# Kernel optimization log

Hardware: AMD Instinct MI355X
Metric: run time of the kernel (lower is better)

## Reference

```python
import jax, jax.numpy as jnp
import numpy as np
from jax import lax

SHIFT_SIZE = 5
PAD = SHIFT_SIZE // 2


def _chunk_shifts(C):
    # torch.chunk(x, 5, dim=1): chunk size = ceil(C/5); shift for chunk i is i - PAD
    csz = -(-C // SHIFT_SIZE)
    return jnp.arange(C) // csz - PAD  # (C,) in [-PAD, PAD]


def _shift_along_h(x, shifts):
    # x: (B,C,H,W). Equivalent of pad+chunk+roll(dim=2)+cat+narrow: per-channel
    # zero-filled shift along H (no wraparound since |shift| <= PAD).
    B, C, H, W = x.shape
    xp = jnp.pad(x, ((0, 0), (0, 0), (PAD, PAD), (0, 0)))
    c_idx = jnp.arange(C)[:, None]              # (C,1)
    h_idx = jnp.arange(H)[None, :] + PAD - shifts[:, None]  # (C,H)
    return xp[:, c_idx, h_idx, :]               # (B,C,H,W)


def _shift_along_w(x, shifts):
    return jnp.swapaxes(_shift_along_h(jnp.swapaxes(x, 2, 3), shifts), 2, 3)


def setup_inputs() -> dict:
    key = jax.random.key(0)
    ks = jax.random.split(key, 7)
    B, H, W, C, hidden = 8, 128, 128, 256, 256
    x = jax.random.normal(ks[0], (B, H * W, C), dtype=jnp.float32)
    w1 = jax.random.normal(ks[1], (hidden, C), dtype=jnp.float32) * 0.02
    b1 = jnp.zeros((hidden,), dtype=jnp.float32)
    fan_out = 3 * 3 * hidden // hidden  # groups = hidden
    dw_w = jax.random.normal(ks[2], (hidden, 1, 3, 3), dtype=jnp.float32) * np.sqrt(2.0 / fan_out)
    dw_b = jnp.zeros((hidden,), dtype=jnp.float32)
    w2 = jax.random.normal(ks[3], (C, hidden), dtype=jnp.float32) * 0.02
    b2 = jnp.zeros((C,), dtype=jnp.float32)
    return {"x": x, "H": H, "W": W, "w1": w1, "b1": b1,
            "dw_w": dw_w, "dw_b": dw_b, "w2": w2, "b2": b2}


def reference(x, H, W, w1, b1, dw_w, dw_b, w2, b2):
    B, N, C = x.shape
    shifts = _chunk_shifts(C)

    # --- shift along H, then fc1 ---
    xn = jnp.reshape(jnp.swapaxes(x, 1, 2), (B, C, H, W))
    x_s = _shift_along_h(xn, shifts)
    x_s = jnp.swapaxes(x_s.reshape(B, C, H * W), 1, 2)   # (B,N,C)
    h = x_s @ w1.T + b1                                  # (B,N,hidden)

    # --- depthwise 3x3 conv ---
    Ch = h.shape[-1]
    himg = jnp.reshape(jnp.swapaxes(h, 1, 2), (B, Ch, H, W))
    himg = lax.conv_general_dilated(
        himg, dw_w, window_strides=(1, 1), padding=((1, 1), (1, 1)),
        feature_group_count=Ch,
        dimension_numbers=("NCHW", "OIHW", "NCHW")) + dw_b[None, :, None, None]
    h = jnp.swapaxes(himg.reshape(B, Ch, H * W), 1, 2)

    h = jax.nn.gelu(h, approximate=False)

    # --- shift along W, then fc2 ---
    hn = jnp.reshape(jnp.swapaxes(h, 1, 2), (B, Ch, H, W))
    h_s = _shift_along_w(hn, _chunk_shifts(Ch))
    h_s = jnp.swapaxes(h_s.reshape(B, Ch, H * W), 1, 2)  # (B,N,hidden)
    out = h_s @ w2.T + b2                                # (B,N,C)
    return out
```

## Files before the change

### kernel.cpp

```cpp
#include <hip/hip_runtime.h>
#include <hip/hip_bf16.h>
#include <math.h>

#define Hc   128
#define Wc   128
#define Cc   256
#define Nc   (Hc * Wc)
#define Bn   8
#define Mtot (Bn * Nc)
#define CSZ  52
#define SPAD 2

typedef unsigned short ushort4v __attribute__((ext_vector_type(4)));
typedef unsigned short ushort8  __attribute__((ext_vector_type(8)));
typedef __bf16         bf16x8   __attribute__((ext_vector_type(8)));
typedef float          f32x4    __attribute__((ext_vector_type(4)));

__device__ __forceinline__ float bf2f(unsigned short u) {
    return __uint_as_float(((unsigned)u) << 16);
}
__device__ __forceinline__ unsigned short f2bf(float f) {
    unsigned u = __float_as_uint(f);
    return (unsigned short)((u + 0x7fffu + ((u >> 16) & 1u)) >> 16);
}
__device__ __forceinline__ unsigned pk2bf(float a, float b) {
    unsigned ua = __float_as_uint(a) + 0x8000u;
    unsigned ub = __float_as_uint(b) + 0x8000u;
    return __builtin_amdgcn_perm(ub, ua, 0x07060302);
}
__device__ __forceinline__ void async16(const void* g, void* l) {
    __builtin_amdgcn_global_load_lds(
        (const __attribute__((address_space(1))) unsigned*)g,
        (__attribute__((address_space(3))) unsigned*)l, 16, 0, 0);
}

__global__ __launch_bounds__(256)
void prep_xshift_kernel(const float* __restrict__ x, unsigned short* __restrict__ xs)
{
    const int gid = blockIdx.x * 256 + threadIdx.x;
    const int grp = gid & 63;
    const int nl  = gid >> 6;
    const int c0  = grp * 4;
    const int s   = c0 / CSZ - SPAD;
    const int h   = (nl & (Nc - 1)) >> 7;
    const int hs  = h - s;
    float4 v = make_float4(0.f, 0.f, 0.f, 0.f);
    if (hs >= 0 && hs < Hc) v = *(const float4*)(x + ((size_t)nl - s * Wc) * Cc + c0);
    ushort4v o = { f2bf(v.x), f2bf(v.y), f2bf(v.z), f2bf(v.w) };
    *(ushort4v*)(xs + (size_t)nl * Cc + c0) = o;
}

__global__ __launch_bounds__(256)
void fc1_mfma_kernel(const unsigned short* __restrict__ A, const float* __restrict__ w1,
                     const float* __restrict__ b1, unsigned short* __restrict__ h1)
{
    __shared__ __bf16 As[128 * 32];
    __shared__ __bf16 Bs[128 * 32];
    __shared__ __align__(16) unsigned short Cs[128 * 136];

    const int tid  = threadIdx.x;
    const int lane = tid & 63;
    const int wave = tid >> 6;
    const int wm = (wave >> 1) * 64, wn = (wave & 1) * 64;
    const size_t m0 = (size_t)blockIdx.x * 128;
    const int j0 = blockIdx.y * 128;

    const int idx0 = tid, idx1 = tid + 256;
    const int brow = tid >> 1, bch = (tid & 1) * 16;

    f32x4 acc[4][4] = {};
    for (int k0 = 0; k0 < Cc; k0 += 32) {
        async16(A + (m0 + (idx0 >> 2)) * Cc + k0 + (idx0 & 3) * 8, As + idx0 * 8);
        async16(A + (m0 + (idx1 >> 2)) * Cc + k0 + (idx1 & 3) * 8, As + idx1 * 8);
        {
            const float* src = w1 + (size_t)(j0 + brow) * Cc + k0 + bch;
            float4 v0 = *(const float4*)(src);
            float4 v1 = *(const float4*)(src + 4);
            float4 v2 = *(const float4*)(src + 8);
            float4 v3 = *(const float4*)(src + 12);
            uint4 p0, p1;
            p0.x = pk2bf(v0.x, v0.y); p0.y = pk2bf(v0.z, v0.w);
            p0.z = pk2bf(v1.x, v1.y); p0.w = pk2bf(v1.z, v1.w);
            p1.x = pk2bf(v2.x, v2.y); p1.y = pk2bf(v2.z, v2.w);
            p1.z = pk2bf(v3.x, v3.y); p1.w = pk2bf(v3.z, v3.w);
            *(uint4*)(Bs + brow * 32 + bch)     = p0;
            *(uint4*)(Bs + brow * 32 + bch + 8) = p1;
        }
        __syncthreads();
        bf16x8 a[4], b[4];
        const int kq = (lane >> 4) * 8;
        const int r  = lane & 15;
#pragma unroll
        for (int i = 0; i < 4; ++i) {
            a[i] = *(const bf16x8*)(As + (wm + i * 16 + r) * 32 + kq);
            b[i] = *(const bf16x8*)(Bs + (wn + i * 16 + r) * 32 + kq);
        }
#pragma unroll
        for (int i = 0; i < 4; ++i)
#pragma unroll
            for (int j = 0; j < 4; ++j)
                acc[i][j] = __builtin_amdgcn_mfma_f32_16x16x32_bf16(a[i], b[j], acc[i][j], 0, 0, 0);
        __syncthreads();
    }

    const int cq = (lane >> 4) * 4;
    const int cc = lane & 15;
    float bv[4];
#pragma unroll
    for (int j = 0; j < 4; ++j) bv[j] = b1[j0 + wn + j * 16 + cc];
#pragma unroll
    for (int i = 0; i < 4; ++i)
#pragma unroll
        for (int j = 0; j < 4; ++j) {
            const int col = wn + j * 16 + cc;
#pragma unroll
            for (int rg = 0; rg < 4; ++rg)
                Cs[(wm + i * 16 + cq + rg) * 136 + col] = f2bf(acc[i][j][rg] + bv[j]);
        }
    __syncthreads();
    {
        const int row = tid >> 1, half = tid & 1;
        const unsigned short* src = Cs + row * 136 + half * 64;
        unsigned short* dst = h1 + (m0 + row) * Cc + j0 + half * 64;
#pragma unroll
        for (int i = 0; i < 8; ++i)
            *(uint4*)(dst + i * 8) = *(const uint4*)(src + i * 8);
    }
}

__global__ __launch_bounds__(256)
void zero_borders_kernel(unsigned short* __restrict__ gsh)
{
    const int gid = blockIdx.x * 256 + threadIdx.x;
    const int cg  = gid & 31;
    const int rest = gid >> 5;
    const int wi = rest & 3;
    const int bh = rest >> 2;
    const int w  = (wi & 2) ? (wi + 124) : wi;
    uint4 z; z.x = z.y = z.z = z.w = 0u;
    *(uint4*)(gsh + ((size_t)bh * 128 + w) * Cc + cg * 8) = z;
}

__global__ __launch_bounds__(256)
void dwconv_gelu_scatter_kernel(const unsigned short* __restrict__ h1,
                                const float* __restrict__ dw_w, const float* __restrict__ dw_b,
                                unsigned short* __restrict__ gsh)
{
    __shared__ float wsm[9][256];
    for (int i = threadIdx.x; i < 9 * 256; i += 256) {
        const int tap = i % 9, c = i / 9;
        wsm[tap][(c >> 3) | ((c & 7) << 5)] = dw_w[i];
    }
    __syncthreads();

    const int n_lin = blockIdx.x * 8 + (threadIdx.x >> 5);
    const int li = threadIdx.x & 31;
    const int cg = li * 8;
    const int b = n_lin >> 14;
    const int n = n_lin & (Nc - 1);
    const int hh = n >> 7, ww = n & 127;
    const size_t bN = (size_t)b * Nc;

    float acc[8];
#pragma unroll
    for (int c = 0; c < 8; ++c) acc[c] = dw_b[cg + c];

#pragma unroll
    for (int dy = -1; dy <= 1; ++dy) {
        const int y = hh + dy;
        if (y < 0 || y >= Hc) continue;
#pragma unroll
        for (int dx = -1; dx <= 1; ++dx) {
            const int xw = ww + dx;
            if (xw < 0 || xw >= Wc) continue;
            const int tap = (dy + 1) * 3 + (dx + 1);
            const ushort8 raw = *(const ushort8*)(h1 + (bN + y * Wc + xw) * Cc + cg);
#pragma unroll
            for (int c = 0; c < 8; ++c)
                acc[c] += bf2f(raw[c]) * wsm[tap][li | (c << 5)];
        }
    }

    unsigned short ov[8];
#pragma unroll
    for (int c = 0; c < 8; ++c) {
        const float v = acc[c];
        ov[c] = f2bf(0.5f * v * (1.0f + erff(v * 0.70710678118654752f)));
    }
    const int s0 = cg / CSZ - SPAD;
    const int s1 = (cg + 4) / CSZ - SPAD;
    const int w0 = ww + s0, w1 = ww + s1;
    if ((unsigned)w0 < (unsigned)Wc) {
        ushort4v t = { ov[0], ov[1], ov[2], ov[3] };
        *(ushort4v*)(gsh + (bN + hh * Wc + w0) * Cc + cg) = t;
    }
    if ((unsigned)w1 < (unsigned)Wc) {
        ushort4v t = { ov[4], ov[5], ov[6], ov[7] };
        *(ushort4v*)(gsh + (bN + hh * Wc + w1) * Cc + cg + 4) = t;
    }
}

__global__ __launch_bounds__(256)
void fc2_mfma_kernel(const unsigned short* __restrict__ A, const float* __restrict__ w2,
                     const float* __restrict__ b2, float* __restrict__ out)
{
    __shared__ __bf16 As[128 * 32];
    __shared__ __bf16 Bs[128 * 32];

    const int tid  = threadIdx.x;
    const int lane = tid & 63;
    const int wave = tid >> 6;
    const int wm = (wave >> 1) * 64, wn = (wave & 1) * 64;
    const size_t m0 = (size_t)blockIdx.x * 128;
    const int j0 = blockIdx.y * 128;

    const int idx0 = tid, idx1 = tid + 256;
    const int brow = tid >> 1, bch = (tid & 1) * 16;

    f32x4 acc[4][4] = {};
    for (int k0 = 0; k0 < Cc; k0 += 32) {
        async16(A + (m0 + (idx0 >> 2)) * Cc + k0 + (idx0 & 3) * 8, As + idx0 * 8);
        async16(A + (m0 + (idx1 >> 2)) * Cc + k0 + (idx1 & 3) * 8, As + idx1 * 8);
        {
            const float* src = w2 + (size_t)(j0 + brow) * Cc + k0 + bch;
            float4 v0 = *(const float4*)(src);
            float4 v1 = *(const float4*)(src + 4);
            float4 v2 = *(const float4*)(src + 8);
            float4 v3 = *(const float4*)(src + 12);
            uint4 p0, p1;
            p0.x = pk2bf(v0.x, v0.y); p0.y = pk2bf(v0.z, v0.w);
            p0.z = pk2bf(v1.x, v1.y); p0.w = pk2bf(v1.z, v1.w);
            p1.x = pk2bf(v2.x, v2.y); p1.y = pk2bf(v2.z, v2.w);
            p1.z = pk2bf(v3.x, v3.y); p1.w = pk2bf(v3.z, v3.w);
            *(uint4*)(Bs + brow * 32 + bch)     = p0;
            *(uint4*)(Bs + brow * 32 + bch + 8) = p1;
        }
        __syncthreads();
        bf16x8 a[4], b[4];
        const int kq = (lane >> 4) * 8;
        const int r  = lane & 15;
#pragma unroll
        for (int i = 0; i < 4; ++i) {
            a[i] = *(const bf16x8*)(As + (wm + i * 16 + r) * 32 + kq);
            b[i] = *(const bf16x8*)(Bs + (wn + i * 16 + r) * 32 + kq);
        }
#pragma unroll
        for (int i = 0; i < 4; ++i)
#pragma unroll
            for (int j = 0; j < 4; ++j)
                acc[i][j] = __builtin_amdgcn_mfma_f32_16x16x32_bf16(a[i], b[j], acc[i][j], 0, 0, 0);
        __syncthreads();
    }

    const int cq = (lane >> 4) * 4;
    const int cc = lane & 15;
    float bv[4];
#pragma unroll
    for (int j = 0; j < 4; ++j) bv[j] = b2[j0 + wn + j * 16 + cc];
#pragma unroll
    for (int i = 0; i < 4; ++i)
#pragma unroll
        for (int j = 0; j < 4; ++j) {
            const int col = j0 + wn + j * 16 + cc;
#pragma unroll
            for (int rg = 0; rg < 4; ++rg)
                out[(m0 + wm + i * 16 + cq + rg) * Cc + col] = acc[i][j][rg] + bv[j];
        }
}

extern "C" void kernel_launch(void* const* d_in, const int* in_sizes, int n_in,
                              void* d_out, int out_size, void* d_ws, size_t ws_size,
                              hipStream_t stream) {
    const float* x    = (const float*)d_in[0];
    const float* w1   = (const float*)d_in[3];
    const float* b1   = (const float*)d_in[4];
    const float* dw_w = (const float*)d_in[5];
    const float* dw_b = (const float*)d_in[6];
    const float* w2   = (const float*)d_in[7];
    const float* b2   = (const float*)d_in[8];
    float* out = (float*)d_out;

    unsigned short* xs  = (unsigned short*)d_ws;
    unsigned short* h1  = xs + (size_t)Mtot * Cc;
    unsigned short* gsh = xs;

    prep_xshift_kernel<<<dim3(Mtot * 64 / 256), dim3(256), 0, stream>>>(x, xs);
    fc1_mfma_kernel<<<dim3(Mtot / 128, 2), dim3(256), 0, stream>>>(xs, w1, b1, h1);
    zero_borders_kernel<<<dim3(512), dim3(256), 0, stream>>>(gsh);
    dwconv_gelu_scatter_kernel<<<dim3(Mtot / 8), dim3(256), 0, stream>>>(h1, dw_w, dw_b, gsh);
    fc2_mfma_kernel<<<dim3(Mtot / 128, 2), dim3(256), 0, stream>>>(gsh, w2, b2, out);
}
```

Before: 418.9 us.

## Fuse H-shift into fc1 A-load, register-block dwconv, and use fast GELU

Drops the separate x-shift prep pass. fc1 now loads fp32 x directly with the per-channel H shift and converts it to bf16 while staging the A tile. A small prep kernel converts w1 to bf16 and transposes the depthwise weights into scratch space inside the output buffer, so fc1 can stream its weights asynchronously. The depthwise conv now computes 4 adjacent output pixels per thread to reuse loaded input columns, and replaces erf-GELU with a tanh-style approximation built from exp and rcp. That approximation changes numerics slightly relative to exact GELU.

Result: faster. 388.5 us (-7.3%).

```diff
diff --git a/kernel.cpp b/kernel.cpp
--- a/kernel.cpp
+++ b/kernel.cpp
@@ -35,23 +35,20 @@
 }
 
 __global__ __launch_bounds__(256)
-void prep_xshift_kernel(const float* __restrict__ x, unsigned short* __restrict__ xs)
-{
-    const int gid = blockIdx.x * 256 + threadIdx.x;
-    const int grp = gid & 63;
-    const int nl  = gid >> 6;
-    const int c0  = grp * 4;
-    const int s   = c0 / CSZ - SPAD;
-    const int h   = (nl & (Nc - 1)) >> 7;
-    const int hs  = h - s;
-    float4 v = make_float4(0.f, 0.f, 0.f, 0.f);
-    if (hs >= 0 && hs < Hc) v = *(const float4*)(x + ((size_t)nl - s * Wc) * Cc + c0);
-    ushort4v o = { f2bf(v.x), f2bf(v.y), f2bf(v.z), f2bf(v.w) };
-    *(ushort4v*)(xs + (size_t)nl * Cc + c0) = o;
-}
-
-__global__ __launch_bounds__(256)
-void fc1_mfma_kernel(const unsigned short* __restrict__ A, const float* __restrict__ w1,
+void wprep_kernel(const float* __restrict__ w1, const float* __restrict__ dw_w,
+                  unsigned short* __restrict__ w1b, float* __restrict__ dwT)
+{
+    const int g = blockIdx.x * 256 + threadIdx.x;
+    {
+        float4 a = *(const float4*)(w1 + (size_t)g * 4);
+        ushort4v o = { f2bf(a.x), f2bf(a.y), f2bf(a.z), f2bf(a.w) };
+        *(ushort4v*)(w1b + (size_t)g * 4) = o;
+    }
+    if (g < 9 * Cc) dwT[(g % 9) * Cc + g / 9] = dw_w[g];
+}
+
+__global__ __launch_bounds__(256)
+void fc1_mfma_kernel(const float* __restrict__ x, const unsigned short* __restrict__ w1b,
                      const float* __restrict__ b1, unsigned short* __restrict__ h1)
 {
     __shared__ __bf16 As[128 * 32];
@@ -62,38 +59,45 @@
     const int lane = tid & 63;
     const int wave = tid >> 6;
     const int wm = (wave >> 1) * 64, wn = (wave & 1) * 64;
-    const size_t m0 = (size_t)blockIdx.x * 128;
+    const int bx = blockIdx.x;
+    const size_t m0 = (size_t)bx * 128;
     const int j0 = blockIdx.y * 128;
-
+    const int bb = bx >> 7, hh = bx & 127;
+    const int r = tid >> 1, half = tid & 1;
     const int idx0 = tid, idx1 = tid + 256;
-    const int brow = tid >> 1, bch = (tid & 1) * 16;
 
     f32x4 acc[4][4] = {};
     for (int k0 = 0; k0 < Cc; k0 += 32) {
-        async16(A + (m0 + (idx0 >> 2)) * Cc + k0 + (idx0 & 3) * 8, As + idx0 * 8);
-        async16(A + (m0 + (idx1 >> 2)) * Cc + k0 + (idx1 & 3) * 8, As + idx1 * 8);
+        async16(w1b + (size_t)(j0 + (idx0 >> 2)) * Cc + k0 + (idx0 & 3) * 8, Bs + idx0 * 8);
+        async16(w1b + (size_t)(j0 + (idx1 >> 2)) * Cc + k0 + (idx1 & 3) * 8, Bs + idx1 * 8);
         {
-            const float* src = w1 + (size_t)(j0 + brow) * Cc + k0 + bch;
-            float4 v0 = *(const float4*)(src);
-            float4 v1 = *(const float4*)(src + 4);
-            float4 v2 = *(const float4*)(src + 8);
-            float4 v3 = *(const float4*)(src + 12);
-            uint4 p0, p1;
-            p0.x = pk2bf(v0.x, v0.y); p0.y = pk2bf(v0.z, v0.w);
-            p0.z = pk2bf(v1.x, v1.y); p0.w = pk2bf(v1.z, v1.w);
-            p1.x = pk2bf(v2.x, v2.y); p1.y = pk2bf(v2.z, v2.w);
-            p1.z = pk2bf(v3.x, v3.y); p1.w = pk2bf(v3.z, v3.w);
-            *(uint4*)(Bs + brow * 32 + bch)     = p0;
-            *(uint4*)(Bs + brow * 32 + bch + 8) = p1;
+            const int kb = k0 + half * 16;
+            unsigned p[8];
+#pragma unroll
+            for (int j = 0; j < 4; ++j) {
+                const int c  = kb + j * 4;
+                const int s  = c / CSZ - SPAD;
+                const int hs = hh - s;
+                float4 v = make_float4(0.f, 0.f, 0.f, 0.f);
+                if (hs >= 0 && hs < Hc)
+                    v = *(const float4*)(x + ((size_t)(bb * Nc + hs * Wc + r)) * Cc + c);
+                p[j * 2]     = pk2bf(v.x, v.y);
+                p[j * 2 + 1] = pk2bf(v.z, v.w);
+            }
+            uint4 q0, q1;
+            q0.x = p[0]; q0.y = p[1]; q0.z = p[2]; q0.w = p[3];
+            q1.x = p[4]; q1.y = p[5]; q1.z = p[6]; q1.w = p[7];
+            *(uint4*)(As + r * 32 + half * 16)     = q0;
+            *(uint4*)(As + r * 32 + half * 16 + 8) = q1;
         }
         __syncthreads();
         bf16x8 a[4], b[4];
         const int kq = (lane >> 4) * 8;
-        const int r  = lane & 15;
+        const int rr = lane & 15;
 #pragma unroll
         for (int i = 0; i < 4; ++i) {
-            a[i] = *(const bf16x8*)(As + (wm + i * 16 + r) * 32 + kq);
-            b[i] = *(const bf16x8*)(Bs + (wn + i * 16 + r) * 32 + kq);
+            a[i] = *(const bf16x8*)(As + (wm + i * 16 + rr) * 32 + kq);
+            b[i] = *(const bf16x8*)(Bs + (wn + i * 16 + rr) * 32 + kq);
         }
 #pragma unroll
         for (int i = 0; i < 4; ++i)
@@ -119,9 +123,9 @@
         }
     __syncthreads();
     {
-        const int row = tid >> 1, half = tid & 1;
-        const unsigned short* src = Cs + row * 136 + half * 64;
-        unsigned short* dst = h1 + (m0 + row) * Cc + j0 + half * 64;
+        const int row = tid >> 1, hf = tid & 1;
+        const unsigned short* src = Cs + row * 136 + hf * 64;
+        unsigned short* dst = h1 + (m0 + row) * Cc + j0 + hf * 64;
 #pragma unroll
         for (int i = 0; i < 8; ++i)
             *(uint4*)(dst + i * 8) = *(const uint4*)(src + i * 8);
@@ -143,60 +147,82 @@
 
 __global__ __launch_bounds__(256)
 void dwconv_gelu_scatter_kernel(const unsigned short* __restrict__ h1,
-                                const float* __restrict__ dw_w, const float* __restrict__ dw_b,
+                                const float* __restrict__ dwT, const float* __restrict__ dw_b,
                                 unsigned short* __restrict__ gsh)
 {
-    __shared__ float wsm[9][256];
-    for (int i = threadIdx.x; i < 9 * 256; i += 256) {
-        const int tap = i % 9, c = i / 9;
-        wsm[tap][(c >> 3) | ((c & 7) << 5)] = dw_w[i];
-    }
-    __syncthreads();
-
-    const int n_lin = blockIdx.x * 8 + (threadIdx.x >> 5);
-    const int li = threadIdx.x & 31;
-    const int cg = li * 8;
-    const int b = n_lin >> 14;
-    const int n = n_lin & (Nc - 1);
-    const int hh = n >> 7, ww = n & 127;
-    const size_t bN = (size_t)b * Nc;
-
-    float acc[8];
-#pragma unroll
-    for (int c = 0; c < 8; ++c) acc[c] = dw_b[cg + c];
+    const int t   = threadIdx.x;
+    const int cg  = t & 31;
+    const int wq  = t >> 5;
+    const int c0  = cg * 8;
+    const int bh  = blockIdx.x >> 2;
+    const int qtr = blockIdx.x & 3;
+    const int bb  = bh >> 7, hh = bh & 127;
+    const size_t rowb = (size_t)bb * Nc + (size_t)hh * Wc;
+    const int wbase = qtr * 32 + wq * 4 - 1;
+
+    float acc[4][8];
+    {
+        float4 a0 = *(const float4*)(dw_b + c0);
+        float4 a1 = *(const float4*)(dw_b + c0 + 4);
+#pragma unroll
+        for (int i = 0; i < 4; ++i) {
+            acc[i][0] = a0.x; acc[i][1] = a0.y; acc[i][2] = a0.z; acc[i][3] = a0.w;
+            acc[i][4] = a1.x; acc[i][5] = a1.y; acc[i][6] = a1.z; acc[i][7] = a1.w;
+        }
+    }
 
 #pragma unroll
     for (int dy = -1; dy <= 1; ++dy) {
         const int y = hh + dy;
         if (y < 0 || y >= Hc) continue;
-#pragma unroll
-        for (int dx = -1; dx <= 1; ++dx) {
-            const int xw = ww + dx;
-            if (xw < 0 || xw >= Wc) continue;
-            const int tap = (dy + 1) * 3 + (dx + 1);
-            const ushort8 raw = *(const ushort8*)(h1 + (bN + y * Wc + xw) * Cc + cg);
-#pragma unroll
-            for (int c = 0; c < 8; ++c)
-                acc[c] += bf2f(raw[c]) * wsm[tap][li | (c << 5)];
-        }
-    }
-
-    unsigned short ov[8];
-#pragma unroll
-    for (int c = 0; c < 8; ++c) {
-        const float v = acc[c];
-        ov[c] = f2bf(0.5f * v * (1.0f + erff(v * 0.70710678118654752f)));
-    }
-    const int s0 = cg / CSZ - SPAD;
-    const int s1 = (cg + 4) / CSZ - SPAD;
-    const int w0 = ww + s0, w1 = ww + s1;
-    if ((unsigned)w0 < (unsigned)Wc) {
-        ushort4v t = { ov[0], ov[1], ov[2], ov[3] };
-        *(ushort4v*)(gsh + (bN + hh * Wc + w0) * Cc + cg) = t;
-    }
-    if ((unsigned)w1 < (unsigned)Wc) {
-        ushort4v t = { ov[4], ov[5], ov[6], ov[7] };
-        *(ushort4v*)(gsh + (bN + hh * Wc + w1) * Cc + cg + 4) = t;
+        const unsigned short* rp = h1 + ((size_t)bb * Nc + (size_t)y * Wc) * Cc + c0;
+        float in[6][8];
+#pragma unroll
+        for (int dx = 0; dx < 6; ++dx) {
+            const int w = wbase + dx;
+            ushort8 raw = {0, 0, 0, 0, 0, 0, 0, 0};
+            if (w >= 0 && w < Wc) raw = *(const ushort8*)(rp + (size_t)w * Cc);
+#pragma unroll
+            for (int c = 0; c < 8; ++c) in[dx][c] = bf2f(raw[c]);
+        }
+        const float* wrow = dwT + (dy + 1) * 3 * Cc + c0;
+        float wr[3][8];
+#pragma unroll
+        for (int tx = 0; tx < 3; ++tx) {
+            float4 wa = *(const float4*)(wrow + tx * Cc);
+            float4 wb = *(const float4*)(wrow + tx * Cc + 4);
+            wr[tx][0] = wa.x; wr[tx][1] = wa.y; wr[tx][2] = wa.z; wr[tx][3] = wa.w;
+            wr[tx][4] = wb.x; wr[tx][5] = wb.y; wr[tx][6] = wb.z; wr[tx][7] = wb.w;
+        }
+#pragma unroll
+        for (int i = 0; i < 4; ++i)
+#pragma unroll
+            for (int tx = 0; tx < 3; ++tx)
+#pragma unroll
+                for (int c = 0; c < 8; ++c)
+                    acc[i][c] += in[i + tx][c] * wr[tx][c];
+    }
+
+    const int s0 = c0 / CSZ - SPAD;
+    const int s1 = (c0 + 4) / CSZ - SPAD;
+#pragma unroll
+    for (int i = 0; i < 4; ++i) {
+        float g[8];
+#pragma unroll
+        for (int c = 0; c < 8; ++c) {
+            const float v = acc[i][c];
+            const float u = v * v;
+            const float a = __builtin_fmaf(0.0713548162f, u, 1.5957691216f);
+            const float e = __expf(v * a);
+            g[c] = v * e * __builtin_amdgcn_rcpf(e + 1.0f);
+        }
+        uint2 lo, hi;
+        lo.x = pk2bf(g[0], g[1]); lo.y = pk2bf(g[2], g[3]);
+        hi.x = pk2bf(g[4], g[5]); hi.y = pk2bf(g[6], g[7]);
+        const int wo = wbase + 1 + i;
+        const int w0 = wo + s0, w1 = wo + s1;
+        if ((unsigned)w0 < (unsigned)Wc) *(uint2*)(gsh + (rowb + w0) * Cc + c0)     = lo;
+        if ((unsigned)w1 < (unsigned)Wc) *(uint2*)(gsh + (rowb + w1) * Cc + c0 + 4) = hi;
     }
 }
 
@@ -238,11 +264,11 @@
         __syncthreads();
         bf16x8 a[4], b[4];
         const int kq = (lane >> 4) * 8;
-        const int r  = lane & 15;
+        const int rr = lane & 15;
 #pragma unroll
         for (int i = 0; i < 4; ++i) {
-            a[i] = *(const bf16x8*)(As + (wm + i * 16 + r) * 32 + kq);
-            b[i] = *(const bf16x8*)(Bs + (wn + i * 16 + r) * 32 + kq);
+            a[i] = *(const bf16x8*)(As + (wm + i * 16 + rr) * 32 + kq);
+            b[i] = *(const bf16x8*)(Bs + (wn + i * 16 + rr) * 32 + kq);
         }
 #pragma unroll
         for (int i = 0; i < 4; ++i)
@@ -280,13 +306,14 @@
     const float* b2   = (const float*)d_in[8];
     float* out = (float*)d_out;
 
-    unsigned short* xs  = (unsigned short*)d_ws;
-    unsigned short* h1  = xs + (size_t)Mtot * Cc;
-    unsigned short* gsh = xs;
-
-    prep_xshift_kernel<<<dim3(Mtot * 64 / 256), dim3(256), 0, stream>>>(x, xs);
-    fc1_mfma_kernel<<<dim3(Mtot / 128, 2), dim3(256), 0, stream>>>(xs, w1, b1, h1);
+    unsigned short* h1  = (unsigned short*)d_ws;
+    unsigned short* gsh = h1 + (size_t)Mtot * Cc;
+    unsigned short* w1b = (unsigned short*)d_out;
+    float*          dwT = (float*)(w1b + 65536);
+
+    wprep_kernel<<<dim3(64), dim3(256), 0, stream>>>(w1, dw_w, w1b, dwT);
+    fc1_mfma_kernel<<<dim3(Mtot / 128, 2), dim3(256), 0, stream>>>(x, w1b, b1, h1);
     zero_borders_kernel<<<dim3(512), dim3(256), 0, stream>>>(gsh);
-    dwconv_gelu_scatter_kernel<<<dim3(Mtot / 8), dim3(256), 0, stream>>>(h1, dw_w, dw_b, gsh);
+    dwconv_gelu_scatter_kernel<<<dim3(4 * Mtot / 128), dim3(256), 0, stream>>>(h1, dwT, dw_b, gsh);
     fc2_mfma_kernel<<<dim3(Mtot / 128, 2), dim3(256), 0, stream>>>(gsh, w2, b2, out);
 }
```
